# Performance work log

Hardware: AMD Instinct MI355X
Metric: run time of the kernel (lower is better)

## Reference

```python
import jax, jax.numpy as jnp
import numpy as np

B, S, D = 4, 2048, 1024
H, Dh = 16, 64


def setup_inputs() -> dict:
    key = jax.random.key(0)
    ks = jax.random.split(key, 9)
    s_in = 1.0 / np.sqrt(D)
    inp = {
        "key": jax.random.normal(ks[0], (B, S, D), jnp.float32),
        "value": jax.random.normal(ks[1], (B, S, D), jnp.float32),
        "query": jax.random.normal(ks[2], (B, S, D), jnp.float32),
        # Linear weights stored as [in, out] (math-equivalent to torch W.T)
        "Wq": jax.random.uniform(ks[3], (D, H * Dh), jnp.float32, -s_in, s_in),
        "bq": jax.random.uniform(ks[4], (H * Dh,), jnp.float32, -s_in, s_in),
        "Wk": jax.random.uniform(ks[5], (D, H * Dh), jnp.float32, -s_in, s_in),
        "bk": jax.random.uniform(ks[6], (H * Dh,), jnp.float32, -s_in, s_in),
        "Wv": jax.random.uniform(ks[7], (D, H * Dh), jnp.float32, -s_in, s_in),
        "bv": jax.random.uniform(ks[8], (H * Dh,), jnp.float32, -s_in, s_in),
    }
    return inp


def reference(key, value, query, Wq, bq, Wk, bk, Wv, bv):
    b, s, _ = key.shape
    # projections -> [B, H, S, Dh]
    q = (query @ Wq + bq).reshape(b, s, H, Dh).transpose(0, 2, 1, 3)
    k = (key @ Wk + bk).reshape(b, s, H, Dh).transpose(0, 2, 1, 3)
    v = (value @ Wv + bv).reshape(b, s, H, Dh).transpose(0, 2, 1, 3)
    scores = jnp.einsum("bhqd,bhkd->bhqk", q, k) / np.sqrt(Dh).astype(np.float32)
    p = jax.nn.softmax(scores, axis=-1)
    out = jnp.einsum("bhqk,bhkd->bhqd", p, v)  # [B, H, S, Dh]
    return out.transpose(0, 2, 1, 3).reshape(b, s, H * Dh)
```

## Files before the change

### kernel.cpp

```cpp
#include <hip/hip_runtime.h>

typedef __bf16 bf16;
typedef __bf16 bf16x8 __attribute__((ext_vector_type(8)));
typedef __bf16 bf16x4 __attribute__((ext_vector_type(4)));
typedef _Float16 f16x4 __attribute__((ext_vector_type(4)));
typedef float  f32x4  __attribute__((ext_vector_type(4)));

#define LOG2E 1.44269504088896340736f
#define SCQ (0.125f * LOG2E)

__device__ __forceinline__ void async16(const void* g, void* l) {
  __builtin_amdgcn_global_load_lds(
      (const __attribute__((address_space(1))) unsigned int*)g,
      (__attribute__((address_space(3))) unsigned int*)l, 16, 0, 0);
}

__device__ __forceinline__ f32x4 mfma_bf16(bf16x8 a, bf16x8 b, f32x4 c) {
  return __builtin_amdgcn_mfma_f32_16x16x32_bf16(a, b, c, 0, 0, 0);
}
__device__ __forceinline__ f32x4 mfma_f16k16(f16x4 a, f16x4 b, f32x4 c) {
  return __builtin_amdgcn_mfma_f32_16x16x16f16(a, b, c, 0, 0, 0);
}

__global__ __launch_bounds__(256) void cvt3(const float* __restrict__ q,
                                            const float* __restrict__ k,
                                            const float* __restrict__ v,
                                            bf16* __restrict__ out) {
  int z = blockIdx.y;
  const float* in = z == 0 ? q : (z == 1 ? k : v);
  bf16* o = out + (size_t)z * 8388608;
  int i = blockIdx.x * 256 + threadIdx.x;
  const float4* p = (const float4*)in;
  float4 a = p[i * 2], c = p[i * 2 + 1];
  bf16x8 r;
  r[0] = (bf16)a.x; r[1] = (bf16)a.y; r[2] = (bf16)a.z; r[3] = (bf16)a.w;
  r[4] = (bf16)c.x; r[5] = (bf16)c.y; r[6] = (bf16)c.z; r[7] = (bf16)c.w;
  ((bf16x8*)o)[i] = r;
}

__global__ __launch_bounds__(256) void wtrans(const float* __restrict__ W0,
                                              const float* __restrict__ W1,
                                              const float* __restrict__ W2,
                                              bf16* __restrict__ Wt) {
  const float* W = blockIdx.z == 0 ? W0 : (blockIdx.z == 1 ? W1 : W2);
  bf16* O = Wt + (size_t)blockIdx.z * (1024 * 1024);
  __shared__ float t[64 * 69];
  int tid = threadIdx.x;
  int k0 = blockIdx.x * 64, n0 = blockIdx.y * 64;
  int r0 = tid >> 4, c0 = (tid & 15) * 4;
#pragma unroll
  for (int rr = 0; rr < 4; rr++) {
    int k = r0 + rr * 16;
    float4 v = *(const float4*)(W + (k0 + k) * 1024 + n0 + c0);
    t[k * 69 + c0 + 0] = v.x; t[k * 69 + c0 + 1] = v.y;
    t[k * 69 + c0 + 2] = v.z; t[k * 69 + c0 + 3] = v.w;
  }
  __syncthreads();
#pragma unroll
  for (int rr = 0; rr < 4; rr++) {
    int n = r0 + rr * 16;
    bf16x4 o;
#pragma unroll
    for (int j = 0; j < 4; j++) o[j] = (bf16)t[(c0 + j) * 69 + n];
    *(bf16x4*)(O + (n0 + n) * 1024 + k0 + c0) = o;
  }
}

__global__ __launch_bounds__(256, 2) void gemm_qkv(const bf16* __restrict__ Act,
                                                   const bf16* __restrict__ Wt,
                                                   const float* __restrict__ b0,
                                                   const float* __restrict__ b1,
                                                   const float* __restrict__ b2,
                                                   bf16* __restrict__ qo,
                                                   bf16* __restrict__ ko,
                                                   _Float16* __restrict__ vf) {
  __shared__ bf16 smem[24576];
  bf16* sA = smem;
  bf16* sB = smem + 8192;
  const int tid = threadIdx.x;
  const int wave = tid >> 6, lane = tid & 63;
  const int quad = lane >> 4, l15 = lane & 15;
  const int z = blockIdx.z;
  const int lin = blockIdx.y * 64 + blockIdx.x;
  const int tx = (lin & 7) | ((lin >> 5) << 3);
  const int ty = (lin >> 3) & 3;
  const int m0 = tx * 128, n0 = ty * 256;
  const bf16* A = Act + (size_t)z * 8388608;
  const bf16* Bt = Wt + (size_t)z * 1048576;
  const float* bias = z == 0 ? b0 : (z == 1 ? b1 : b2);

  const bf16* ap[4]; int loa[4];
  const bf16* bp[8]; int lob[8];
#pragma unroll
  for (int i = 0; i < 4; i++) {
    int g = wave * 256 + i * 64 + lane;
    int row = g >> 3, jl = (g & 7) ^ (row & 7);
    ap[i] = A + (m0 + row) * 1024 + jl * 8;
    loa[i] = (wave * 256 + i * 64) * 8;
  }
#pragma unroll
  for (int i = 0; i < 8; i++) {
    int g = wave * 512 + i * 64 + lane;
    int row = g >> 3, jl = (g & 7) ^ (row & 7);
    bp[i] = Bt + (n0 + row) * 1024 + jl * 8;
    lob[i] = (wave * 512 + i * 64) * 8;
  }
  const int wm = (wave & 1) * 64, wn = (wave >> 1) * 128;
  f32x4 acc[4][8] = {};

  for (int kt = 0; kt < 16; kt++) {
    const int ko_ = kt * 64;
#pragma unroll
    for (int i = 0; i < 4; i++) async16(ap[i] + ko_, sA + loa[i]);
#pragma unroll
    for (int i = 0; i < 8; i++) async16(bp[i] + ko_, sB + lob[i]);
    __syncthreads();
#pragma unroll
    for (int ks = 0; ks < 2; ks++) {
      bf16x8 af[4];
#pragma unroll
      for (int mt = 0; mt < 4; mt++) {
        int m = wm + mt * 16 + l15;
        int ph = (ks * 4 + quad) ^ (m & 7);
        af[mt] = *(const bf16x8*)(sA + m * 64 + ph * 8);
      }
#pragma unroll
      for (int nh = 0; nh < 2; nh++) {
        bf16x8 bv[4];
#pragma unroll
        for (int nt = 0; nt < 4; nt++) {
          int n = wn + (nh * 4 + nt) * 16 + l15;
          int ph = (ks * 4 + quad) ^ (n & 7);
          bv[nt] = *(const bf16x8*)(sB + n * 64 + ph * 8);
        }
#pragma unroll
        for (int mt = 0; mt < 4; mt++)
#pragma unroll
          for (int nt = 0; nt < 4; nt++)
            acc[mt][nh * 4 + nt] = mfma_bf16(af[mt], bv[nt], acc[mt][nh * 4 + nt]);
      }
    }
    __syncthreads();
  }

  if (z != 2) {
    bf16* O = z == 0 ? qo : ko;
    const float sc = z == 0 ? SCQ : 1.0f;
#pragma unroll
    for (int nt = 0; nt < 8; nt++) {
      int n = n0 + wn + nt * 16 + l15;
      float bc = bias[n];
#pragma unroll
      for (int mt = 0; mt < 4; mt++)
#pragma unroll
        for (int r = 0; r < 4; r++) {
          int m = m0 + wm + mt * 16 + quad * 4 + r;
          O[m * 1024 + n] = (bf16)((acc[mt][nt][r] + bc) * sc);
        }
    }
  } else {
    const int b = m0 >> 11, s0 = m0 & 2047;
    const int kvb = (s0 + wm) >> 6;
#pragma unroll
    for (int nt = 0; nt < 8; nt++) {
      int nn = n0 + wn + nt * 16;
      int h = nn >> 6, dt = (nn >> 4) & 3;
      float bc = bias[nn + l15];
#pragma unroll
      for (int mt = 0; mt < 4; mt++) {
        f16x4 pk;
#pragma unroll
        for (int r = 0; r < 4; r++) pk[r] = (_Float16)(acc[mt][nt][r] + bc);
        size_t off = ((((size_t)(b * 16 + h) * 32 + kvb) * 16 + (mt * 4 + dt)) * 64 + lane) * 4;
        *(f16x4*)(vf + off) = pk;
      }
    }
  }
}

__global__ __launch_bounds__(256, 4) void attn(const bf16* __restrict__ Q,
                                               const bf16* __restrict__ K,
                                               const _Float16* __restrict__ VF,
                                               float* __restrict__ Out) {
  __shared__ bf16 sQ[8192];
  __shared__ bf16 sK[8192];
  __shared__ _Float16 sV[8192];
  const int tid = threadIdx.x;
  const int wave = tid >> 6, lane = tid & 63;
  const int quad = lane >> 4, l15 = lane & 15;
  const int q0 = blockIdx.x * 128, h = blockIdx.y, b = blockIdx.z;
  const bf16* Kbase = K + (size_t)(b * 2048) * 1024 + h * 64;
  const _Float16* Vbase = VF + (size_t)(b * 16 + h) * 131072;

#pragma unroll
  for (int i = 0; i < 4; i++) {
    int g = i * 256 + tid;
    int row = g >> 3, jl = (g & 7) ^ (row & 7);
    async16(Q + (size_t)(b * 2048 + q0 + row) * 1024 + h * 64 + jl * 8, sQ + g * 8);
    async16(Kbase + (size_t)row * 1024 + jl * 8, sK + g * 8);
    async16(Vbase + g * 8, sV + g * 8);
  }
  __syncthreads();

  bf16x8 qf[2][2];
#pragma unroll
  for (int qt2 = 0; qt2 < 2; qt2++)
#pragma unroll
    for (int ks = 0; ks < 2; ks++) {
      int m = wave * 32 + qt2 * 16 + l15;
      int ph = (ks * 4 + quad) ^ (l15 & 7);
      qf[qt2][ks] = *(const bf16x8*)(sQ + m * 64 + ph * 8);
    }

  f32x4 oaccT[2][4] = {};
  float ls[2] = {0.f, 0.f};
  const int ph0 = quad ^ (l15 & 7), ph1 = (4 + quad) ^ (l15 & 7);

  for (int kvb = 0; kvb < 16; kvb++) {
#pragma unroll
    for (int t = 0; t < 8; t++) {
      int row = t * 16 + l15;
      bf16x8 kf0 = *(const bf16x8*)(sK + row * 64 + ph0 * 8);
      bf16x8 kf1 = *(const bf16x8*)(sK + row * 64 + ph1 * 8);
      f32x4 st0 = {}, st1 = {};
      st0 = mfma_bf16(kf0, qf[0][0], st0);
      st0 = mfma_bf16(kf1, qf[0][1], st0);
      st1 = mfma_bf16(kf0, qf[1][0], st1);
      st1 = mfma_bf16(kf1, qf[1][1], st1);
      f16x4 pf0, pf1;
#pragma unroll
      for (int r = 0; r < 4; r++) {
        float p0 = __builtin_amdgcn_exp2f(st0[r]);
        float p1 = __builtin_amdgcn_exp2f(st1[r]);
        ls[0] += p0; ls[1] += p1;
        pf0[r] = (_Float16)p0; pf1[r] = (_Float16)p1;
      }
      const _Float16* sVt = sV + (t >> 2) * 4096;
      int tl = (t & 3) * 4;
#pragma unroll
      for (int dt = 0; dt < 4; dt++) {
        f16x4 va = *(const f16x4*)(sVt + ((tl + dt) * 64 + lane) * 4);
        oaccT[0][dt] = mfma_f16k16(va, pf0, oaccT[0][dt]);
        oaccT[1][dt] = mfma_f16k16(va, pf1, oaccT[1][dt]);
      }
    }
    __syncthreads();
    if (kvb < 15) {
      int kn = (kvb + 1) * 128;
#pragma unroll
      for (int i = 0; i < 4; i++) {
        int g = i * 256 + tid;
        int row = g >> 3, jl = (g & 7) ^ (row & 7);
        async16(Kbase + (size_t)(kn + row) * 1024 + jl * 8, sK + g * 8);
        async16(Vbase + (kvb + 1) * 8192 + g * 8, sV + g * 8);
      }
      __syncthreads();
    }
  }

#pragma unroll
  for (int qt2 = 0; qt2 < 2; qt2++) {
    float l = ls[qt2];
    l += __shfl_xor(l, 16);
    l += __shfl_xor(l, 32);
    float inv = 1.f / l;
    int qrow = b * 2048 + q0 + wave * 32 + qt2 * 16 + l15;
#pragma unroll
    for (int dt = 0; dt < 4; dt++) {
      float4 v;
      v.x = oaccT[qt2][dt][0] * inv;
      v.y = oaccT[qt2][dt][1] * inv;
      v.z = oaccT[qt2][dt][2] * inv;
      v.w = oaccT[qt2][dt][3] * inv;
      *(float4*)(Out + (size_t)qrow * 1024 + h * 64 + dt * 16 + quad * 4) = v;
    }
  }
}

extern "C" void kernel_launch(void* const* d_in, const int* in_sizes, int n_in,
                              void* d_out, int out_size, void* d_ws, size_t ws_size,
                              hipStream_t stream) {
  const float* key   = (const float*)d_in[0];
  const float* value = (const float*)d_in[1];
  const float* query = (const float*)d_in[2];
  const float* Wq = (const float*)d_in[3];
  const float* bq = (const float*)d_in[4];
  const float* Wk = (const float*)d_in[5];
  const float* bk = (const float*)d_in[6];
  const float* Wv = (const float*)d_in[7];
  const float* bv = (const float*)d_in[8];
  float* out = (float*)d_out;

  char* ws = (char*)d_ws;
  bf16* actb   = (bf16*)(ws);
  bf16* wt     = (bf16*)(ws + 50331648);
  bf16* qo     = (bf16*)(ws + 56623104);
  bf16* ko     = (bf16*)(ws + 73400320);
  _Float16* vf = (_Float16*)(ws + 90177536);
  (void)in_sizes; (void)n_in; (void)out_size; (void)ws_size;

  wtrans<<<dim3(16, 16, 3), 256, 0, stream>>>(Wq, Wk, Wv, wt);
  cvt3<<<dim3(4096, 3), 256, 0, stream>>>(query, key, value, actb);
  gemm_qkv<<<dim3(64, 4, 3), 256, 0, stream>>>(actb, wt, bq, bk, bv, qo, ko, vf);
  attn<<<dim3(16, 16, 4), 256, 0, stream>>>(qo, ko, vf, out);
}
```

Baseline: 314.0 us.

## Double-buffer K/V tiles in attention and widen V fragment loads

New measurement: 333.3 us. +6.1%, slower.

```diff
diff --git a/kernel.cpp b/kernel.cpp
--- a/kernel.cpp
+++ b/kernel.cpp
@@ -4,6 +4,7 @@
 typedef __bf16 bf16x8 __attribute__((ext_vector_type(8)));
 typedef __bf16 bf16x4 __attribute__((ext_vector_type(4)));
 typedef _Float16 f16x4 __attribute__((ext_vector_type(4)));
+typedef _Float16 f16x8 __attribute__((ext_vector_type(8)));
 typedef float  f32x4  __attribute__((ext_vector_type(4)));
 
 #define LOG2E 1.44269504088896340736f
@@ -160,19 +161,23 @@
     }
   } else {
     const int b = m0 >> 11, s0 = m0 & 2047;
-    const int kvb = (s0 + wm) >> 6;
-#pragma unroll
-    for (int nt = 0; nt < 8; nt++) {
-      int nn = n0 + wn + nt * 16;
-      int h = nn >> 6, dt = (nn >> 4) & 3;
-      float bc = bias[nn + l15];
+    const int kvb64 = (s0 + wm) >> 6;
+#pragma unroll
+    for (int k2 = 0; k2 < 4; k2++) {
+      int nn = n0 + wn + k2 * 32;
+      int h = nn >> 6, np = (nn >> 5) & 1;
+      float bc0 = bias[nn + l15];
+      float bc1 = bias[nn + 16 + l15];
 #pragma unroll
       for (int mt = 0; mt < 4; mt++) {
-        f16x4 pk;
-#pragma unroll
-        for (int r = 0; r < 4; r++) pk[r] = (_Float16)(acc[mt][nt][r] + bc);
-        size_t off = ((((size_t)(b * 16 + h) * 32 + kvb) * 16 + (mt * 4 + dt)) * 64 + lane) * 4;
-        *(f16x4*)(vf + off) = pk;
+        f16x8 pk;
+#pragma unroll
+        for (int r = 0; r < 4; r++) {
+          pk[r]     = (_Float16)(acc[mt][2 * k2][r] + bc0);
+          pk[4 + r] = (_Float16)(acc[mt][2 * k2 + 1][r] + bc1);
+        }
+        size_t off = ((((size_t)(b * 16 + h) * 32 + kvb64) * 8 + (mt * 2 + np)) * 64 + lane) * 8;
+        *(f16x8*)(vf + off) = pk;
       }
     }
   }
@@ -183,8 +188,8 @@
                                                const _Float16* __restrict__ VF,
                                                float* __restrict__ Out) {
   __shared__ bf16 sQ[8192];
-  __shared__ bf16 sK[8192];
-  __shared__ _Float16 sV[8192];
+  __shared__ bf16 sK[2][4096];
+  __shared__ _Float16 sV[2][4096];
   const int tid = threadIdx.x;
   const int wave = tid >> 6, lane = tid & 63;
   const int quad = lane >> 4, l15 = lane & 15;
@@ -197,8 +202,13 @@
     int g = i * 256 + tid;
     int row = g >> 3, jl = (g & 7) ^ (row & 7);
     async16(Q + (size_t)(b * 2048 + q0 + row) * 1024 + h * 64 + jl * 8, sQ + g * 8);
-    async16(Kbase + (size_t)row * 1024 + jl * 8, sK + g * 8);
-    async16(Vbase + g * 8, sV + g * 8);
+  }
+#pragma unroll
+  for (int i = 0; i < 2; i++) {
+    int g = i * 256 + tid;
+    int row = g >> 3, jl = (g & 7) ^ (row & 7);
+    async16(Kbase + (size_t)row * 1024 + jl * 8, sK[0] + g * 8);
+    async16(Vbase + g * 8, sV[0] + g * 8);
   }
   __syncthreads();
 
@@ -216,12 +226,27 @@
   float ls[2] = {0.f, 0.f};
   const int ph0 = quad ^ (l15 & 7), ph1 = (4 + quad) ^ (l15 & 7);
 
-  for (int kvb = 0; kvb < 16; kvb++) {
-#pragma unroll
-    for (int t = 0; t < 8; t++) {
+  for (int kvb = 0; kvb < 32; kvb++) {
+    const int cur = kvb & 1;
+    if (kvb < 31) {
+      int kn = (kvb + 1) * 64;
+      bf16* dK = sK[cur ^ 1];
+      _Float16* dV = sV[cur ^ 1];
+#pragma unroll
+      for (int i = 0; i < 2; i++) {
+        int g = i * 256 + tid;
+        int row = g >> 3, jl = (g & 7) ^ (row & 7);
+        async16(Kbase + (size_t)(kn + row) * 1024 + jl * 8, dK + g * 8);
+        async16(Vbase + (kvb + 1) * 4096 + g * 8, dV + g * 8);
+      }
+    }
+    const bf16* sKc = sK[cur];
+    const _Float16* sVc = sV[cur];
+#pragma unroll
+    for (int t = 0; t < 4; t++) {
       int row = t * 16 + l15;
-      bf16x8 kf0 = *(const bf16x8*)(sK + row * 64 + ph0 * 8);
-      bf16x8 kf1 = *(const bf16x8*)(sK + row * 64 + ph1 * 8);
+      bf16x8 kf0 = *(const bf16x8*)(sKc + row * 64 + ph0 * 8);
+      bf16x8 kf1 = *(const bf16x8*)(sKc + row * 64 + ph1 * 8);
       f32x4 st0 = {}, st1 = {};
       st0 = mfma_bf16(kf0, qf[0][0], st0);
       st0 = mfma_bf16(kf1, qf[0][1], st0);
@@ -235,25 +260,20 @@
         ls[0] += p0; ls[1] += p1;
         pf0[r] = (_Float16)p0; pf1[r] = (_Float16)p1;
       }
-      const _Float16* sVt = sV + (t >> 2) * 4096;
-      int tl = (t & 3) * 4;
-#pragma unroll
-      for (int dt = 0; dt < 4; dt++) {
-        f16x4 va = *(const f16x4*)(sVt + ((tl + dt) * 64 + lane) * 4);
-        oaccT[0][dt] = mfma_f16k16(va, pf0, oaccT[0][dt]);
-        oaccT[1][dt] = mfma_f16k16(va, pf1, oaccT[1][dt]);
-      }
-    }
-    __syncthreads();
-    if (kvb < 15) {
-      int kn = (kvb + 1) * 128;
-#pragma unroll
-      for (int i = 0; i < 4; i++) {
-        int g = i * 256 + tid;
-        int row = g >> 3, jl = (g & 7) ^ (row & 7);
-        async16(Kbase + (size_t)(kn + row) * 1024 + jl * 8, sK + g * 8);
-        async16(Vbase + (kvb + 1) * 8192 + g * 8, sV + g * 8);
-      }
+      const _Float16* sVt = sVc + t * 1024;
+#pragma unroll
+      for (int np = 0; np < 2; np++) {
+        f16x8 va2 = *(const f16x8*)(sVt + np * 512 + lane * 8);
+        f16x4 lo = __builtin_shufflevector(va2, va2, 0, 1, 2, 3);
+        f16x4 hi = __builtin_shufflevector(va2, va2, 4, 5, 6, 7);
+        oaccT[0][2 * np]     = mfma_f16k16(lo, pf0, oaccT[0][2 * np]);
+        oaccT[0][2 * np + 1] = mfma_f16k16(hi, pf0, oaccT[0][2 * np + 1]);
+        oaccT[1][2 * np]     = mfma_f16k16(lo, pf1, oaccT[1][2 * np]);
+        oaccT[1][2 * np + 1] = mfma_f16k16(hi, pf1, oaccT[1][2 * np + 1]);
+      }
+    }
+    if (kvb < 31) {
+      __builtin_amdgcn_s_waitcnt(0);
       __syncthreads();
     }
   }
```
